# Performance work log

Measured on AMD Instinct MI355X. Metric: run time of the kernel, lower is better.

The kernel has to match this reference:

```python
import jax, jax.numpy as jnp
import numpy as np

N_NODES = 50000
N_EDGES = 800000
IN_CH = 128
HID_CH = 256
N_GRAPHS = 500


def setup_inputs() -> dict:
    key = jax.random.key(0)
    k = jax.random.split(key, 8)
    x = jax.random.normal(k[0], (N_NODES, IN_CH), dtype=jnp.float32)
    edge_index = jax.random.randint(k[1], (2, N_EDGES), 0, N_NODES, dtype=jnp.int32)
    batch = jnp.sort(jax.random.randint(k[2], (N_NODES,), 0, N_GRAPHS, dtype=jnp.int32))
    # GCNConv weights (glorot-ish scaling) and zero biases, Linear fc is unused in forward
    W1 = jax.random.normal(k[3], (IN_CH, HID_CH), dtype=jnp.float32) / np.sqrt(IN_CH)
    b1 = jnp.zeros((HID_CH,), dtype=jnp.float32)
    W2 = jax.random.normal(k[4], (HID_CH, HID_CH), dtype=jnp.float32) / np.sqrt(HID_CH)
    b2 = jnp.zeros((HID_CH,), dtype=jnp.float32)
    return {"x": x, "W1": W1, "b1": b1, "W2": W2, "b2": b2,
            "edge_index": edge_index, "batch": batch}


def _gcn_conv(x, W, b, src, dst, norm, n_nodes):
    # x' = scatter_add_dst( norm_e * (x @ W)[src] ) + b   (self-loops already in src/dst)
    xw = x @ W                              # [N, H]
    msg = xw[src] * norm[:, None]           # [E+N, H]
    out = jax.ops.segment_sum(msg, dst, num_segments=n_nodes)
    return out + b


def reference(x, W1, b1, W2, b2, edge_index, batch):
    n = x.shape[0]
    # add self-loops (PyG GCNConv default)
    loop = jnp.arange(n, dtype=edge_index.dtype)
    src = jnp.concatenate([edge_index[0], loop])
    dst = jnp.concatenate([edge_index[1], loop])
    # symmetric normalization D^{-1/2} (A+I) D^{-1/2}; deg from dst counts
    deg = jax.ops.segment_sum(jnp.ones_like(dst, dtype=x.dtype), dst, num_segments=n)
    dis = jnp.where(deg > 0, jax.lax.rsqrt(deg), 0.0)
    norm = dis[src] * dis[dst]              # [E+N]

    h = jax.nn.relu(_gcn_conv(x, W1, b1, src, dst, norm, n))
    h = jax.nn.relu(_gcn_conv(h, W2, b2, src, dst, norm, n))

    # global_mean_pool over batch ids
    sums = jax.ops.segment_sum(h, batch, num_segments=N_GRAPHS)
    cnts = jax.ops.segment_sum(jnp.ones((n,), dtype=h.dtype), batch, num_segments=N_GRAPHS)
    return sums / jnp.maximum(cnts, 1.0)[:, None]
```

## Files before the change

kernel.cpp:

```cpp
#include <hip/hip_runtime.h>

#define HID 256
#define SLOTS 30
#define OVCAP 16384
typedef unsigned short ushort_t;
typedef unsigned int uint_t;
typedef __attribute__((ext_vector_type(8))) short short8;
typedef __attribute__((ext_vector_type(4))) float f32x4;
typedef __attribute__((ext_vector_type(4))) unsigned short us4;
typedef __attribute__((ext_vector_type(8))) unsigned short us8;

__device__ __forceinline__ ushort_t f2b(float f) {
    uint_t u = __float_as_uint(f);
    u = u + 0x7fffu + ((u >> 16) & 1u);
    return (ushort_t)(u >> 16);
}

__global__ __launch_bounds__(256) void k_cfprep(const int* __restrict__ src,
                                                const int* __restrict__ dstp,
                                                ushort_t* __restrict__ csr2,
                                                int* __restrict__ ovn,
                                                int2* __restrict__ ov, int E,
                                                const float* __restrict__ W1,
                                                ushort_t* __restrict__ Wt1,
                                                const float* __restrict__ W2,
                                                ushort_t* __restrict__ Wt2,
                                                int eb, int p1b, int p2b) {
    int bid = blockIdx.x;
    if (bid < eb) {
        int i = bid * 256 + threadIdx.x;
        if (i >= E) return;
        int d = dstp[i], s = src[i];
        int* rowcnt = (int*)(csr2 + (size_t)d * 32) + 15;
        int c = atomicAdd(rowcnt, 1);
        if (c < SLOTS) {
            csr2[(size_t)d * 32 + c] = (ushort_t)s;
        } else {
            int p = atomicAdd(ovn, 1);
            if (p < OVCAP) ov[p] = make_int2(d, s);
        }
        return;
    }
    const float* W = (bid < eb + p1b) ? W1 : W2;
    ushort_t* Wt = (bid < eb + p1b) ? Wt1 : Wt2;
    int kg = (bid < eb + p1b) ? (bid - eb) : (bid - eb - p1b);
    int c = threadIdx.x;
    float v = W[(size_t)kg * HID + c];
    int p = kg >> 6;
    int k = kg & 63;
    int byte_ = c * 128 + k * 2;
    int slot = byte_ >> 4;
    int sw = (slot & ~7) | ((slot ^ c) & 7);
    size_t dst_byte = (size_t)p * 32768 + ((size_t)sw << 4) + (byte_ & 15);
    Wt[dst_byte >> 1] = f2b(v);
}

__global__ __launch_bounds__(256) void k_castdis(const float* __restrict__ x,
                                                 const ushort_t* __restrict__ csr2,
                                                 ushort_t* __restrict__ xg,
                                                 float* __restrict__ dis,
                                                 int n, int rshift) {
    int i = blockIdx.x * 256 + threadIdx.x;
    int total8 = n << rshift;
    if (i >= total8) return;
    int r = i >> rshift;
    int j = i & ((1 << rshift) - 1);
    int deg = ((const int*)csr2)[r * 16 + 15];
    float dv = rsqrtf((float)(deg + 1));
    if (j == 0) dis[r] = dv;
    const float4* p = (const float4*)(x + (size_t)i * 8);
    float4 v0 = p[0], v1 = p[1];
    us8 o;
    o[0] = f2b(v0.x * dv); o[1] = f2b(v0.y * dv); o[2] = f2b(v0.z * dv); o[3] = f2b(v0.w * dv);
    o[4] = f2b(v1.x * dv); o[5] = f2b(v1.y * dv); o[6] = f2b(v1.z * dv); o[7] = f2b(v1.w * dv);
    size_t dst = (size_t)(j >> 2) * ((size_t)n * 32) + (size_t)r * 32 + (size_t)(j & 3) * 8;
    *(us8*)(xg + dst) = o;
}

#define ACC8(r)                                                            \
    a0 += __uint_as_float((r).x << 16); a1 += __uint_as_float((r).x & 0xffff0000u); \
    a2 += __uint_as_float((r).y << 16); a3 += __uint_as_float((r).y & 0xffff0000u); \
    a4 += __uint_as_float((r).z << 16); a5 += __uint_as_float((r).z & 0xffff0000u); \
    a6 += __uint_as_float((r).w << 16); a7 += __uint_as_float((r).w & 0xffff0000u);

#define ACC8B(r)                                                           \
    b0 += __uint_as_float((r).x << 16); b1 += __uint_as_float((r).x & 0xffff0000u); \
    b2 += __uint_as_float((r).y << 16); b3 += __uint_as_float((r).y & 0xffff0000u); \
    b4 += __uint_as_float((r).z << 16); b5 += __uint_as_float((r).z & 0xffff0000u); \
    b6 += __uint_as_float((r).w << 16); b7 += __uint_as_float((r).w & 0xffff0000u);

template <int NG>
__global__ __launch_bounds__(256) void k_agg_g(const ushort_t* __restrict__ Yg,
                                               ushort_t* __restrict__ Z,
                                               const ushort_t* __restrict__ csr2,
                                               const int* __restrict__ ovn,
                                               const int2* __restrict__ ov,
                                               const float* __restrict__ dis, int n) {
    const int LOG = (NG == 8) ? 3 : 2;
    const int g = blockIdx.x & (NG - 1);
    const int chunk = blockIdx.x >> LOG;
    const int q = threadIdx.x >> 4;
    const int l16 = threadIdx.x & 15;
    const int par = l16 >> 2;
    const int sub = l16 & 3;
    const int v0 = chunk * 32 + q * 2;
    if (v0 >= n) return;
    const int v1 = v0 + 1;
    const bool has1 = (v1 < n);
    const uint4* Yb = (const uint4*)(Yg + (size_t)g * ((size_t)n * 32));
    const ushort_t* rowb0 = csr2 + (size_t)v0 * 32;
    const ushort_t* rowb1 = csr2 + (size_t)v1 * 32;
    const int deg0 = ((const int*)rowb0)[15];
    const int deg1 = has1 ? ((const int*)rowb1)[15] : 0;
    const int lim0 = min(deg0, SLOTS);
    const int lim1 = min(deg1, SLOTS);
    const int base = par * 8;
    us8 idx0 = *(const us8*)(rowb0 + base);
    us8 idx1 = {};
    if (has1) idx1 = *(const us8*)(rowb1 + base);
    uint4 self0 = make_uint4(0u, 0u, 0u, 0u), self1 = make_uint4(0u, 0u, 0u, 0u);
    if (par == 0) self0 = Yb[(uint_t)v0 * 4u + sub];
    if (has1 && par == 1) self1 = Yb[(uint_t)v1 * 4u + sub];

    const bool g0 = base < lim0;
    const bool g1 = has1 && (base < lim1);
    uint4 r0, r1, r2, r3, r4, r5, r6, r7;
    uint4 s0, s1, s2, s3, s4, s5, s6, s7;
    if (g0) {
        r0 = Yb[(uint_t)idx0[0] * 4u + sub]; r1 = Yb[(uint_t)idx0[1] * 4u + sub];
        r2 = Yb[(uint_t)idx0[2] * 4u + sub]; r3 = Yb[(uint_t)idx0[3] * 4u + sub];
        r4 = Yb[(uint_t)idx0[4] * 4u + sub]; r5 = Yb[(uint_t)idx0[5] * 4u + sub];
        r6 = Yb[(uint_t)idx0[6] * 4u + sub]; r7 = Yb[(uint_t)idx0[7] * 4u + sub];
    }
    if (g1) {
        s0 = Yb[(uint_t)idx1[0] * 4u + sub]; s1 = Yb[(uint_t)idx1[1] * 4u + sub];
        s2 = Yb[(uint_t)idx1[2] * 4u + sub]; s3 = Yb[(uint_t)idx1[3] * 4u + sub];
        s4 = Yb[(uint_t)idx1[4] * 4u + sub]; s5 = Yb[(uint_t)idx1[5] * 4u + sub];
        s6 = Yb[(uint_t)idx1[6] * 4u + sub]; s7 = Yb[(uint_t)idx1[7] * 4u + sub];
    }
    float a0 = 0.f, a1 = 0.f, a2 = 0.f, a3 = 0.f, a4 = 0.f, a5 = 0.f, a6 = 0.f, a7 = 0.f;
    float b0 = 0.f, b1 = 0.f, b2 = 0.f, b3 = 0.f, b4 = 0.f, b5 = 0.f, b6 = 0.f, b7 = 0.f;
    if (g0) {
        if (base + 0 < lim0) { ACC8(r0); }
        if (base + 1 < lim0) { ACC8(r1); }
        if (base + 2 < lim0) { ACC8(r2); }
        if (base + 3 < lim0) { ACC8(r3); }
        if (base + 4 < lim0) { ACC8(r4); }
        if (base + 5 < lim0) { ACC8(r5); }
        if (base + 6 < lim0) { ACC8(r6); }
        if (base + 7 < lim0) { ACC8(r7); }
    }
    if (g1) {
        if (base + 0 < lim1) { ACC8B(s0); }
        if (base + 1 < lim1) { ACC8B(s1); }
        if (base + 2 < lim1) { ACC8B(s2); }
        if (base + 3 < lim1) { ACC8B(s3); }
        if (base + 4 < lim1) { ACC8B(s4); }
        if (base + 5 < lim1) { ACC8B(s5); }
        if (base + 6 < lim1) { ACC8B(s6); }
        if (base + 7 < lim1) { ACC8B(s7); }
    }
    if (deg0 > SLOTS) {
        int m = min(*ovn, OVCAP);
        for (int i2 = par; i2 < m; i2 += 4) {
            int2 p = ov[i2];
            if (p.x == v0) { uint4 r = Yb[(uint_t)p.y * 4u + sub]; ACC8(r); }
        }
    }
    if (deg1 > SLOTS) {
        int m = min(*ovn, OVCAP);
        for (int i2 = par; i2 < m; i2 += 4) {
            int2 p = ov[i2];
            if (p.x == v1) { uint4 r = Yb[(uint_t)p.y * 4u + sub]; ACC8B(r); }
        }
    }
    a0 += __shfl_xor(a0, 4, 64); a1 += __shfl_xor(a1, 4, 64);
    a2 += __shfl_xor(a2, 4, 64); a3 += __shfl_xor(a3, 4, 64);
    a4 += __shfl_xor(a4, 4, 64); a5 += __shfl_xor(a5, 4, 64);
    a6 += __shfl_xor(a6, 4, 64); a7 += __shfl_xor(a7, 4, 64);
    a0 += __shfl_xor(a0, 8, 64); a1 += __shfl_xor(a1, 8, 64);
    a2 += __shfl_xor(a2, 8, 64); a3 += __shfl_xor(a3, 8, 64);
    a4 += __shfl_xor(a4, 8, 64); a5 += __shfl_xor(a5, 8, 64);
    a6 += __shfl_xor(a6, 8, 64); a7 += __shfl_xor(a7, 8, 64);
    b0 += __shfl_xor(b0, 4, 64); b1 += __shfl_xor(b1, 4, 64);
    b2 += __shfl_xor(b2, 4, 64); b3 += __shfl_xor(b3, 4, 64);
    b4 += __shfl_xor(b4, 4, 64); b5 += __shfl_xor(b5, 4, 64);
    b6 += __shfl_xor(b6, 4, 64); b7 += __shfl_xor(b7, 4, 64);
    b0 += __shfl_xor(b0, 8, 64); b1 += __shfl_xor(b1, 8, 64);
    b2 += __shfl_xor(b2, 8, 64); b3 += __shfl_xor(b3, 8, 64);
    b4 += __shfl_xor(b4, 8, 64); b5 += __shfl_xor(b5, 8, 64);
    b6 += __shfl_xor(b6, 8, 64); b7 += __shfl_xor(b7, 8, 64);
    if (par == 0) {
        ACC8(self0);
        float dv = dis[v0];
        us8 o;
        o[0] = f2b(a0 * dv); o[1] = f2b(a1 * dv); o[2] = f2b(a2 * dv); o[3] = f2b(a3 * dv);
        o[4] = f2b(a4 * dv); o[5] = f2b(a5 * dv); o[6] = f2b(a6 * dv); o[7] = f2b(a7 * dv);
        us8* zp = (us8*)(Z + (size_t)v0 * (NG * 32) + g * 32 + sub * 8);
        __builtin_nontemporal_store(o, zp);
    }
    if (has1 && par == 1) {
        ACC8B(self1);
        float dv = dis[v1];
        us8 o;
        o[0] = f2b(b0 * dv); o[1] = f2b(b1 * dv); o[2] = f2b(b2 * dv); o[3] = f2b(b3 * dv);
        o[4] = f2b(b4 * dv); o[5] = f2b(b5 * dv); o[6] = f2b(b6 * dv); o[7] = f2b(b7 * dv);
        us8* zp = (us8*)(Z + (size_t)v1 * (NG * 32) + g * 32 + sub * 8);
        __builtin_nontemporal_store(o, zp);
    }
}

template <int K, bool SCALE, bool OUTG>
__global__ __launch_bounds__(512) void k_gemm_mfma(const ushort_t* __restrict__ A,
                                                   const ushort_t* __restrict__ Wt,
                                                   const float* __restrict__ dis,
                                                   const float* __restrict__ bias,
                                                   ushort_t* __restrict__ Yout, int M) {
    __shared__ char lds[49152];
    char* As = lds;
    char* Bs = lds + 16384;
    const int tid = threadIdx.x;
    const int lane = tid & 63;
    const int w = tid >> 6;
    const int wm = w & 1;
    const int wn = w >> 1;
    const int row0 = blockIdx.x * 128;

    f32x4 acc[4][4];
#pragma unroll
    for (int i = 0; i < 4; ++i)
#pragma unroll
        for (int j = 0; j < 4; ++j) acc[i][j] = (f32x4){0.f, 0.f, 0.f, 0.f};

    for (int k0 = 0; k0 < K; k0 += 64) {
#pragma unroll
        for (int q = 0; q < 2; ++q) {
            int s = q * 512 + tid;
            int r = s >> 3;
            int kseg = (s & 7) ^ (r & 7);
            int row = row0 + r;
            if (row >= M) row = 0;
            const ushort_t* g = A + (size_t)row * K + k0 + kseg * 8;
            __builtin_amdgcn_global_load_lds((const uint_t*)g,
                                             (uint_t*)(As + q * 8192 + w * 1024), 16, 0, 0);
        }
        const ushort_t* gp = Wt + (size_t)(k0 >> 6) * (256 * 64);
#pragma unroll
        for (int q = 0; q < 4; ++q) {
            int s = q * 512 + tid;
            __builtin_amdgcn_global_load_lds((const uint_t*)(gp + (size_t)s * 8),
                                             (uint_t*)(Bs + q * 8192 + w * 1024), 16, 0, 0);
        }
        __syncthreads();
#pragma unroll
        for (int k32 = 0; k32 < 2; ++k32) {
            const int ksl = k32 * 4 + (lane >> 4);
            short8 wf[4], xf[4];
#pragma unroll
            for (int nn = 0; nn < 4; ++nn) {
                int col = wn * 64 + nn * 16 + (lane & 15);
                int slot = col * 8 + (ksl ^ (col & 7));
                wf[nn] = *(const short8*)(Bs + slot * 16);
            }
#pragma unroll
            for (int m = 0; m < 4; ++m) {
                int row = wm * 64 + m * 16 + (lane & 15);
                int slot = row * 8 + (ksl ^ (row & 7));
                xf[m] = *(const short8*)(As + slot * 16);
            }
#pragma unroll
            for (int nn = 0; nn < 4; ++nn)
#pragma unroll
                for (int m = 0; m < 4; ++m)
                    acc[nn][m] = __builtin_amdgcn_mfma_f32_16x16x32_bf16(wf[nn], xf[m],
                                                                         acc[nn][m], 0, 0, 0);
        }
        __syncthreads();
    }
    const int m_lo = lane & 15, c_hi = lane >> 4;
#pragma unroll
    for (int m = 0; m < 4; ++m) {
        int row = row0 + wm * 64 + m * 16 + m_lo;
        if (row < M) {
            float dv = SCALE ? dis[row] : 1.f;
#pragma unroll
            for (int nn = 0; nn < 4; ++nn) {
                int c0 = wn * 64 + nn * 16 + c_hi * 4;
                float4 bb = *(const float4*)(bias + c0);
                us4 o;
                o[0] = f2b(fmaxf(acc[nn][m][0] + bb.x, 0.f) * dv);
                o[1] = f2b(fmaxf(acc[nn][m][1] + bb.y, 0.f) * dv);
                o[2] = f2b(fmaxf(acc[nn][m][2] + bb.z, 0.f) * dv);
                o[3] = f2b(fmaxf(acc[nn][m][3] + bb.w, 0.f) * dv);
                size_t dst = OUTG
                    ? ((size_t)(c0 >> 5) * ((size_t)M * 32) + (size_t)row * 32 + (c0 & 31))
                    : ((size_t)row * HID + c0);
                *(us4*)(Yout + dst) = o;
            }
        }
    }
}

__global__ __launch_bounds__(256) void k_pool2(const ushort_t* __restrict__ H,
                                               const int* __restrict__ batch,
                                               float* __restrict__ out, int n) {
    __shared__ int se[2];
    int g = blockIdx.x;
    if (threadIdx.x < 2) {
        int tgt = g + (int)threadIdx.x;
        int lo = 0, hi = n;
        while (lo < hi) { int mid = (lo + hi) >> 1; if (batch[mid] < tgt) lo = mid + 1; else hi = mid; }
        se[threadIdx.x] = lo;
    }
    __syncthreads();
    int s = se[0], e = se[1];
    int c = threadIdx.x;
    float sum = 0.f;
    for (int i = s; i < e; ++i)
        sum += __uint_as_float(((uint_t)H[(size_t)i * HID + c]) << 16);
    out[(size_t)g * HID + c] = sum / (float)max(e - s, 1);
}

extern "C" void kernel_launch(void* const* d_in, const int* in_sizes, int n_in,
                              void* d_out, int out_size, void* d_ws, size_t ws_size,
                              hipStream_t stream) {
    const float* x = (const float*)d_in[0];
    const float* W1 = (const float*)d_in[1];
    const float* b1 = (const float*)d_in[2];
    const float* W2 = (const float*)d_in[3];
    const float* b2 = (const float*)d_in[4];
    const int* ei = (const int*)d_in[5];
    const int* batch = (const int*)d_in[6];
    float* out = (float*)d_out;

    const int N = in_sizes[6];
    const int E = in_sizes[5] / 2;
    const int K1 = in_sizes[0] / N;
    const int G = out_size / HID;
    (void)n_in; (void)ws_size;

    char* w = (char*)d_ws;
    int* ovn = (int*)(w + 0);
    int2* ov = (int2*)(w + 64);
    ushort_t* csr2 = (ushort_t*)(w + 131136);
    float* dis = (float*)(w + 3331136);
    ushort_t* Wt1 = (ushort_t*)(w + 3531136);
    ushort_t* Wt2 = (ushort_t*)(w + 3596672);
    ushort_t* Xg = (ushort_t*)(w + 3727744);
    ushort_t* Z1 = (ushort_t*)(w + 16527744);
    ushort_t* H1g = (ushort_t*)(w + 29327744);
    ushort_t* Z2 = (ushort_t*)(w + 3727744);
    ushort_t* H2 = (ushort_t*)(w + 29327744);

    hipMemsetAsync(w, 0, 3331136, stream);

    const int eb = (E + 255) / 256;
    k_cfprep<<<eb + K1 + HID, 256, 0, stream>>>(ei, ei + E, csr2, ovn, ov, E,
                                                W1, Wt1, W2, Wt2, eb, K1, HID);

    int rshift = 31 - __builtin_clz((unsigned)(K1 / 8));
    int castb = (N * K1 / 8 + 255) / 256;
    k_castdis<<<castb, 256, 0, stream>>>(x, csr2, Xg, dis, N, rshift);

    int gblk = (N + 127) / 128;
    const int chunks32 = (N + 31) / 32;
    k_agg_g<4><<<4 * chunks32, 256, 0, stream>>>(Xg, Z1, csr2, ovn, ov, dis, N);
    k_gemm_mfma<128, true, true><<<gblk, 512, 0, stream>>>(Z1, Wt1, dis, b1, H1g, N);
    k_agg_g<8><<<8 * chunks32, 256, 0, stream>>>(H1g, Z2, csr2, ovn, ov, dis, N);
    k_gemm_mfma<256, false, false><<<gblk, 512, 0, stream>>>(Z2, Wt2, dis, b2, H2, N);

    k_pool2<<<G, 256, 0, stream>>>(H2, batch, out, N);
}
```

Before: 216.9 us.

## Build CSR via bucketed counting sort instead of global atomics

Replaces the per-edge global atomicAdd CSR build with a three-pass counting sort: a per-block histogram over 256-node buckets, a scan, then a scatter into bucket-ordered packed pairs. A per-bucket kernel then assembles rows in shared memory, writes them coalesced, and computes dis. The aim is to remove contended global atomics, scattered 2-byte writes and the large memset. In exchange it adds three extra launches, including a single-block serial scan, plus extra edge passes through global memory.

```diff
diff --git a/kernel.cpp b/kernel.cpp
--- a/kernel.cpp
+++ b/kernel.cpp
@@ -3,6 +3,7 @@
 #define HID 256
 #define SLOTS 30
 #define OVCAP 16384
+#define NB 256
 typedef unsigned short ushort_t;
 typedef unsigned int uint_t;
 typedef __attribute__((ext_vector_type(8))) short short8;
@@ -16,35 +17,32 @@
     return (ushort_t)(u >> 16);
 }
 
-__global__ __launch_bounds__(256) void k_cfprep(const int* __restrict__ src,
-                                                const int* __restrict__ dstp,
-                                                ushort_t* __restrict__ csr2,
-                                                int* __restrict__ ovn,
-                                                int2* __restrict__ ov, int E,
-                                                const float* __restrict__ W1,
-                                                ushort_t* __restrict__ Wt1,
-                                                const float* __restrict__ W2,
-                                                ushort_t* __restrict__ Wt2,
-                                                int eb, int p1b, int p2b) {
+__global__ __launch_bounds__(256) void k_histprep(const int* __restrict__ dst,
+                                                  int* __restrict__ hist,
+                                                  int E, int CH, int NBKT,
+                                                  const float* __restrict__ W1,
+                                                  ushort_t* __restrict__ Wt1,
+                                                  const float* __restrict__ W2,
+                                                  ushort_t* __restrict__ Wt2, int p1b) {
     int bid = blockIdx.x;
-    if (bid < eb) {
-        int i = bid * 256 + threadIdx.x;
-        if (i >= E) return;
-        int d = dstp[i], s = src[i];
-        int* rowcnt = (int*)(csr2 + (size_t)d * 32) + 15;
-        int c = atomicAdd(rowcnt, 1);
-        if (c < SLOTS) {
-            csr2[(size_t)d * 32 + c] = (ushort_t)s;
-        } else {
-            int p = atomicAdd(ovn, 1);
-            if (p < OVCAP) ov[p] = make_int2(d, s);
-        }
+    int tid = threadIdx.x;
+    if (bid < NB) {
+        __shared__ int h[256];
+        h[tid] = 0;
+        __syncthreads();
+        int e0 = bid * CH;
+        for (int it = tid; it < CH; it += 256) {
+            int e = e0 + it;
+            if (e < E) atomicAdd(&h[dst[e] >> 8], 1);
+        }
+        __syncthreads();
+        if (tid < NBKT) hist[tid * NB + bid] = h[tid];
         return;
     }
-    const float* W = (bid < eb + p1b) ? W1 : W2;
-    ushort_t* Wt = (bid < eb + p1b) ? Wt1 : Wt2;
-    int kg = (bid < eb + p1b) ? (bid - eb) : (bid - eb - p1b);
-    int c = threadIdx.x;
+    const float* W = (bid < NB + p1b) ? W1 : W2;
+    ushort_t* Wt = (bid < NB + p1b) ? Wt1 : Wt2;
+    int kg = (bid < NB + p1b) ? (bid - NB) : (bid - NB - p1b);
+    int c = tid;
     float v = W[(size_t)kg * HID + c];
     int p = kg >> 6;
     int k = kg & 63;
@@ -55,19 +53,110 @@
     Wt[dst_byte >> 1] = f2b(v);
 }
 
+__global__ __launch_bounds__(256) void k_scanb(const int* __restrict__ hist,
+                                               int* __restrict__ offb,
+                                               int* __restrict__ base, int NBKT) {
+    __shared__ int s[256];
+    int t = threadIdx.x;
+    int sum = 0;
+    if (t < NBKT) {
+        const int* hp = hist + t * NB;
+        for (int blk = 0; blk < NB; ++blk) sum += hp[blk];
+    }
+    s[t] = sum;
+    __syncthreads();
+#pragma unroll
+    for (int d = 1; d < 256; d <<= 1) {
+        int u = (t >= d) ? s[t - d] : 0;
+        __syncthreads();
+        s[t] += u;
+        __syncthreads();
+    }
+    int myBase = s[t] - sum;
+    if (t < NBKT) {
+        base[t] = myBase;
+        int run = myBase;
+        const int* hp = hist + t * NB;
+        int* op = offb + t * NB;
+        for (int blk = 0; blk < NB; ++blk) { op[blk] = run; run += hp[blk]; }
+    }
+    if (t == 255) base[NBKT] = s[255];
+}
+
+__global__ __launch_bounds__(256) void k_scatter(const int* __restrict__ src,
+                                                 const int* __restrict__ dst,
+                                                 const int* __restrict__ offb,
+                                                 uint_t* __restrict__ scat,
+                                                 int E, int CH) {
+    __shared__ int h[256];
+    int tid = threadIdx.x;
+    int bid = blockIdx.x;
+    h[tid] = 0;
+    __syncthreads();
+    int e0 = bid * CH;
+    for (int it = tid; it < CH; it += 256) {
+        int e = e0 + it;
+        if (e < E) {
+            int d = dst[e], sv = src[e];
+            int b = d >> 8;
+            int r = atomicAdd(&h[b], 1);
+            scat[offb[b * NB + bid] + r] = ((uint_t)sv << 8) | (uint_t)(d & 255);
+        }
+    }
+}
+
+__global__ __launch_bounds__(256) void k_csr(const uint_t* __restrict__ scat,
+                                             const int* __restrict__ base,
+                                             ushort_t* __restrict__ csr2,
+                                             float* __restrict__ dis,
+                                             int* __restrict__ ovn,
+                                             int2* __restrict__ ov, int n) {
+    __shared__ ushort_t rows[256 * 32];
+    __shared__ int rc[256];
+    int tid = threadIdx.x;
+    int b = blockIdx.x;
+    rc[tid] = 0;
+    uint4* r4 = (uint4*)rows;
+#pragma unroll
+    for (int k = tid; k < 1024; k += 256) r4[k] = make_uint4(0u, 0u, 0u, 0u);
+    __syncthreads();
+    int lo = base[b], hi = base[b + 1];
+    for (int i = lo + tid; i < hi; i += 256) {
+        uint_t p = scat[i];
+        int local = (int)(p & 255u);
+        int sv = (int)(p >> 8);
+        int c = atomicAdd(&rc[local], 1);
+        if (c < SLOTS) {
+            rows[local * 32 + c] = (ushort_t)sv;
+        } else {
+            int q = atomicAdd(ovn, 1);
+            if (q < OVCAP) ov[q] = make_int2(b * 256 + local, sv);
+        }
+    }
+    __syncthreads();
+    ((int*)(rows + tid * 32))[15] = rc[tid];
+    int node = b * 256 + tid;
+    if (node < n) dis[node] = rsqrtf((float)(rc[tid] + 1));
+    __syncthreads();
+    int node0 = b * 256;
+    uint4* cg = (uint4*)csr2;
+#pragma unroll
+    for (int k = tid; k < 1024; k += 256) {
+        int row = k >> 2, word = k & 3;
+        if (node0 + row < n) cg[(size_t)(node0 + row) * 4 + word] = r4[row * 4 + word];
+    }
+}
+
 __global__ __launch_bounds__(256) void k_castdis(const float* __restrict__ x,
-                                                 const ushort_t* __restrict__ csr2,
+                                                 const float* __restrict__ dis,
                                                  ushort_t* __restrict__ xg,
-                                                 float* __restrict__ dis,
                                                  int n, int rshift) {
     int i = blockIdx.x * 256 + threadIdx.x;
     int total8 = n << rshift;
     if (i >= total8) return;
     int r = i >> rshift;
     int j = i & ((1 << rshift) - 1);
-    int deg = ((const int*)csr2)[r * 16 + 15];
-    float dv = rsqrtf((float)(deg + 1));
-    if (j == 0) dis[r] = dv;
+    float dv = dis[r];
     const float4* p = (const float4*)(x + (size_t)i * 8);
     float4 v0 = p[0], v1 = p[1];
     us8 o;
@@ -351,16 +440,24 @@
     ushort_t* H1g = (ushort_t*)(w + 29327744);
     ushort_t* Z2 = (ushort_t*)(w + 3727744);
     ushort_t* H2 = (ushort_t*)(w + 29327744);
-
-    hipMemsetAsync(w, 0, 3331136, stream);
-
-    const int eb = (E + 255) / 256;
-    k_cfprep<<<eb + K1 + HID, 256, 0, stream>>>(ei, ei + E, csr2, ovn, ov, E,
-                                                W1, Wt1, W2, Wt2, eb, K1, HID);
+    int* hist = (int*)(w + 54927744);
+    int* offb = (int*)(w + 55128448);
+    int* base = (int*)(w + 55329152);
+    uint_t* scat = (uint_t*)(w + 55330048);
+
+    hipMemsetAsync(ovn, 0, 64, stream);
+
+    const int NBKT = (N + 255) >> 8;
+    const int CH = (E + NB - 1) / NB;
+    k_histprep<<<NB + K1 + HID, 256, 0, stream>>>(ei + E, hist, E, CH, NBKT,
+                                                  W1, Wt1, W2, Wt2, K1);
+    k_scanb<<<1, 256, 0, stream>>>(hist, offb, base, NBKT);
+    k_scatter<<<NB, 256, 0, stream>>>(ei, ei + E, offb, scat, E, CH);
+    k_csr<<<NBKT, 256, 0, stream>>>(scat, base, csr2, dis, ovn, ov, N);
 
     int rshift = 31 - __builtin_clz((unsigned)(K1 / 8));
     int castb = (N * K1 / 8 + 255) / 256;
-    k_castdis<<<castb, 256, 0, stream>>>(x, csr2, Xg, dis, N, rshift);
+    k_castdis<<<castb, 256, 0, stream>>>(x, dis, Xg, N, rshift);
 
     int gblk = (N + 127) / 128;
     const int chunks32 = (N + 31) / 32;
```

Result: faster. 208.9 us (-3.7%).
